# Performance work log

Measured on AMD Instinct MI355X. Metric: run time of the kernel, lower is better.

The kernel has to match this reference:

```python
import jax, jax.numpy as jnp
import numpy as np

EPS = 1e-9
# ((top,bottom),(left,right)) zero-pads for the 8 neighbor directions,
# matching torch nn.ZeroPad2d((l,r,t,b)) order gate1..gate8 in the source.
PADS = [((0, 2), (0, 2)), ((0, 2), (1, 1)), ((0, 2), (2, 0)),
        ((1, 1), (0, 2)), ((1, 1), (2, 0)),
        ((2, 0), (0, 2)), ((2, 0), (1, 1)), ((2, 0), (2, 0))]


def _pad8(x):
    # x: (B,H,W) -> (B,8,H+2,W+2): 8 directional zero-padded shifts
    return jnp.stack([jnp.pad(x, ((0, 0), tb, lr)) for tb, lr in PADS], axis=1)


def _affinity_normalization(guidance):
    # guidance: (B,8,H,W) -> gate_wb (B,8,H+2,W+2), gate_sum (B,H,W)
    gate_wb = jnp.stack(
        [jnp.pad(guidance[:, k], ((0, 0), tb, lr)) for k, (tb, lr) in enumerate(PADS)],
        axis=1)
    abs_weight = jnp.sum(jnp.abs(gate_wb), axis=1, keepdims=True)
    gate_wb = gate_wb / (abs_weight + EPS)
    gate_sum = jnp.sum(gate_wb, axis=1)[:, 1:-1, 1:-1]
    return gate_wb, gate_sum


def setup_inputs() -> dict:
    key = jax.random.key(0)
    k1, k2, k3, k4 = jax.random.split(key, 4)
    B, H, W = 2, 384, 1280
    guidance = jax.random.normal(k1, (B, 8, H, W), dtype=jnp.float32)
    blur_depth = jax.random.uniform(k2, (B, 1, H, W), dtype=jnp.float32) * 80.0
    valid = (jax.random.uniform(k3, (B, 1, H, W)) < 0.05).astype(jnp.float32)
    sparse_depth = valid * jax.random.uniform(k4, (B, 1, H, W), dtype=jnp.float32) * 80.0
    return {"guidance": guidance, "blur_depth": blur_depth,
            "sparse_depth": sparse_depth, "prop_time": 24}


def reference(guidance, blur_depth, sparse_depth, prop_time):
    # CSPN affinity-guided iterative propagation (norm_type='8sum')
    gate_wb, gate_sum = _affinity_normalization(guidance)
    raw = blur_depth[:, 0]                       # (B,H,W)
    sparse_mask = jnp.sign(sparse_depth[:, 0])   # (B,H,W), 1 where valid
    d = raw
    for _ in range(prop_time):
        # weighted sum over 8 padded neighbor shifts, then crop halo
        nws = jnp.sum(gate_wb * _pad8(d), axis=1)[:, 1:-1, 1:-1]
        d = (1.0 - gate_sum) * raw + nws
        d = (1.0 - sparse_mask) * d + sparse_mask * raw
    return d  # (B,H,W), matches result_depth.squeeze(1)
```

## Files before the change

### kernel.cpp

```cpp
#include <hip/hip_runtime.h>
#include <hip/hip_fp16.h>

static constexpr int Hh = 384;
static constexpr int Ww = 1280;
static constexpr int HW = Hh * Ww;
static constexpr int NPIX = 2 * HW;
static constexpr int TILE_I = 24;
static constexpr int TILE_J = 40;
static constexpr int S_STEPS = 8;
static constexpr int RI = TILE_I + 2 * S_STEPS;
static constexpr int RJ = TILE_J + 2 * S_STEPS;
static constexpr int RR = RI * RJ;
static constexpr int II = RI - 2;
static constexpr int IJ = RJ - 2;
static constexpr int NPAIR_ROW = IJ / 2;
static constexpr int NPAIR = II * NPAIR_ROW;
static constexpr int BLOCK = 512;
static constexpr int PPQ = (RR + BLOCK - 1) / BLOCK;
static constexpr int PPR = (NPAIR + BLOCK - 1) / BLOCK;
static constexpr int TI_T = Hh / TILE_I;
static constexpr int TJ_T = Ww / TILE_J;
static constexpr int GRID = 2 * TI_T * TJ_T;
static constexpr int NXCD = 8;
static constexpr int CHUNK = GRID / NXCD;
static constexpr float EPSF = 1e-9f;

static constexpr int DI[8] = { 1, 1, 1, 0, 0, -1, -1, -1 };
static constexpr int DJ[8] = { 1, 0, -1, 1, -1, 1, 0, -1 };

static __device__ __forceinline__ int iclamp(int v, int lo, int hi) {
    return min(max(v, lo), hi);
}

template <bool FIRST>
__global__ __launch_bounds__(BLOCK, 4)
void mega(
    const float* __restrict__ g,
    const float* blur,
    const float* __restrict__ sparse,
    const float* din,
    float* __restrict__ dout)
{
    __shared__ float sd[2][RR];

    const int tid = threadIdx.x;
    int bx = ((int)blockIdx.x % NXCD) * CHUNK + (int)blockIdx.x / NXCD;
    const int tj = bx % TJ_T; bx /= TJ_T;
    const int ti = bx % TI_T;
    const int b  = bx / TI_T;
    const int oi = ti * TILE_I - S_STEPS;
    const int oj = tj * TILE_J - S_STEPS;

    const float* blurb = blur + (size_t)b * HW;
    const float* dinb  = (FIRST ? blur : din) + (size_t)b * HW;
    const float* gb    = g + (size_t)b * 8 * HW;

#pragma unroll
    for (int q = 0; q < PPQ; q++) {
        int p = tid + q * BLOCK;
        if (p < RR) {
            int ri = p / RJ, rj = p - ri * RJ;
            int gi = iclamp(oi + ri, 0, Hh - 1);
            int gj = iclamp(oj + rj, 0, Ww - 1);
            sd[0][p] = dinb[gi * Ww + gj];
        }
    }

    __half2 wp[PPR][8];
    float2  Cc[PPR];
    int     pr[PPR];
#pragma unroll
    for (int q = 0; q < PPR; q++) {
        int pi = tid + q * BLOCK;
        if (pi < NPAIR) {
            int r0 = pi / NPAIR_ROW;
            int c0 = pi - r0 * NPAIR_ROW;
            int ri = 1 + r0;
            int rj = 1 + 2 * c0;
            int p  = ri * RJ + rj;
            int rngr = min(ri, RI - 1 - ri);
            int rng0 = min(rngr, min(rj,     RJ - 1 - rj));
            int rng1 = min(rngr, min(rj + 1, RJ - 2 - rj));
            pr[q] = p | (max(rng0, rng1) << 16);
            float Cv[2], wv[2][8];
#pragma unroll
            for (int x = 0; x < 2; x++) {
                int gi = iclamp(oi + ri, 0, Hh - 1);
                int gj = iclamp(oj + rj + x, 0, Ww - 1);
                float v[8];
                float a = EPSF;
#pragma unroll
                for (int k = 0; k < 8; k++) {
                    int ii = gi + DI[k], jj = gj + DJ[k];
                    float gv = 0.0f;
                    if (ii >= 0 && ii < Hh && jj >= 0 && jj < Ww)
                        gv = gb[k * HW + ii * Ww + jj];
                    v[k] = gv;
                    a += fabsf(gv);
                }
                float inv = 1.0f / a, gs = 0.0f;
#pragma unroll
                for (int k = 0; k < 8; k++) { v[k] *= inv; gs += v[k]; }
                int idx = gi * Ww + gj;
                float rawv = blurb[idx];
                bool m = sparse[b * HW + idx] > 0.0f;
                Cv[x] = m ? rawv : (1.0f - gs) * rawv;
#pragma unroll
                for (int k = 0; k < 8; k++) wv[x][k] = m ? 0.0f : v[k];
            }
            Cc[q] = make_float2(Cv[0], Cv[1]);
#pragma unroll
            for (int k = 0; k < 8; k++)
                wp[q][k] = __halves2half2(__float2half(wv[0][k]),
                                          __float2half(wv[1][k]));
        } else {
            pr[q] = 0;
            Cc[q] = make_float2(0.0f, 0.0f);
#pragma unroll
            for (int k = 0; k < 8; k++)
                wp[q][k] = __halves2half2(__float2half(0.0f), __float2half(0.0f));
        }
    }
    __syncthreads();

    int cur = 0;
#pragma unroll 1
    for (int s = 1; s < S_STEPS; ++s) {
        const float* s0 = sd[cur];
        float* s1 = sd[cur ^ 1];
#pragma unroll
        for (int q = 0; q < PPR; q++) {
            if ((pr[q] >> 16) >= s) {
                int p = pr[q] & 0xffff;
                float2 uA = *(const float2*)(s0 + p - RJ - 1);
                float2 uB = *(const float2*)(s0 + p - RJ + 1);
                float2 mA = *(const float2*)(s0 + p - 1);
                float2 mB = *(const float2*)(s0 + p + 1);
                float2 dA = *(const float2*)(s0 + p + RJ - 1);
                float2 dB = *(const float2*)(s0 + p + RJ + 1);
                float ax = Cc[q].x, ay = Cc[q].y;
                ax = fmaf(__low2float (wp[q][0]), dB.x, ax);
                ay = fmaf(__high2float(wp[q][0]), dB.y, ay);
                ax = fmaf(__low2float (wp[q][1]), dA.y, ax);
                ay = fmaf(__high2float(wp[q][1]), dB.x, ay);
                ax = fmaf(__low2float (wp[q][2]), dA.x, ax);
                ay = fmaf(__high2float(wp[q][2]), dA.y, ay);
                ax = fmaf(__low2float (wp[q][3]), mB.x, ax);
                ay = fmaf(__high2float(wp[q][3]), mB.y, ay);
                ax = fmaf(__low2float (wp[q][4]), mA.x, ax);
                ay = fmaf(__high2float(wp[q][4]), mA.y, ay);
                ax = fmaf(__low2float (wp[q][5]), uB.x, ax);
                ay = fmaf(__high2float(wp[q][5]), uB.y, ay);
                ax = fmaf(__low2float (wp[q][6]), uA.y, ax);
                ay = fmaf(__high2float(wp[q][6]), uB.x, ay);
                ax = fmaf(__low2float (wp[q][7]), uA.x, ax);
                ay = fmaf(__high2float(wp[q][7]), uA.y, ay);
                s1[p]     = ax;
                s1[p + 1] = ay;
            }
        }
        __syncthreads();
        cur ^= 1;
    }

    const float* s0 = sd[cur];
#pragma unroll
    for (int q = 0; q < PPR; q++) {
        if ((pr[q] >> 16) >= S_STEPS) {
            int p = pr[q] & 0xffff;
            float2 uA = *(const float2*)(s0 + p - RJ - 1);
            float2 uB = *(const float2*)(s0 + p - RJ + 1);
            float2 mA = *(const float2*)(s0 + p - 1);
            float2 mB = *(const float2*)(s0 + p + 1);
            float2 dA = *(const float2*)(s0 + p + RJ - 1);
            float2 dB = *(const float2*)(s0 + p + RJ + 1);
            float ax = Cc[q].x, ay = Cc[q].y;
            ax = fmaf(__low2float (wp[q][0]), dB.x, ax);
            ay = fmaf(__high2float(wp[q][0]), dB.y, ay);
            ax = fmaf(__low2float (wp[q][1]), dA.y, ax);
            ay = fmaf(__high2float(wp[q][1]), dB.x, ay);
            ax = fmaf(__low2float (wp[q][2]), dA.x, ax);
            ay = fmaf(__high2float(wp[q][2]), dA.y, ay);
            ax = fmaf(__low2float (wp[q][3]), mB.x, ax);
            ay = fmaf(__high2float(wp[q][3]), mB.y, ay);
            ax = fmaf(__low2float (wp[q][4]), mA.x, ax);
            ay = fmaf(__high2float(wp[q][4]), mA.y, ay);
            ax = fmaf(__low2float (wp[q][5]), uB.x, ax);
            ay = fmaf(__high2float(wp[q][5]), uB.y, ay);
            ax = fmaf(__low2float (wp[q][6]), uA.y, ax);
            ay = fmaf(__high2float(wp[q][6]), uB.x, ay);
            ax = fmaf(__low2float (wp[q][7]), uA.x, ax);
            ay = fmaf(__high2float(wp[q][7]), uA.y, ay);
            int ri = p / RJ, rj = p - ri * RJ;
            int gbase = b * HW + (oi + ri) * Ww + (oj + rj);
            if (rj >= S_STEPS && rj < RJ - S_STEPS)
                dout[gbase]     = ax;
            if (rj + 1 >= S_STEPS && rj + 1 < RJ - S_STEPS)
                dout[gbase + 1] = ay;
        }
    }
}

extern "C" void kernel_launch(void* const* d_in, const int* in_sizes, int n_in,
                              void* d_out, int out_size, void* d_ws, size_t ws_size,
                              hipStream_t stream) {
    const float* guidance = (const float*)d_in[0];
    const float* blur     = (const float*)d_in[1];
    const float* sparse   = (const float*)d_in[2];
    float* out = (float*)d_out;

    char* ws = (char*)d_ws;
    float* bufA = (float*)ws;
    float* bufB = bufA + NPIX;

    mega<true ><<<GRID, BLOCK, 0, stream>>>(guidance, blur, sparse, nullptr, bufA);
    mega<false><<<GRID, BLOCK, 0, stream>>>(guidance, blur, sparse, bufA, bufB);
    mega<false><<<GRID, BLOCK, 0, stream>>>(guidance, blur, sparse, bufB, out);
}
```

Measured before the change: 149.2 us.

## Precompute normalized affinity weights once in a separate kernel and enlarge tiles

```diff
diff --git a/kernel.cpp b/kernel.cpp
--- a/kernel.cpp
+++ b/kernel.cpp
@@ -5,7 +5,7 @@
 static constexpr int Ww = 1280;
 static constexpr int HW = Hh * Ww;
 static constexpr int NPIX = 2 * HW;
-static constexpr int TILE_I = 24;
+static constexpr int TILE_I = 32;
 static constexpr int TILE_J = 40;
 static constexpr int S_STEPS = 8;
 static constexpr int RI = TILE_I + 2 * S_STEPS;
@@ -25,19 +25,56 @@
 static constexpr int CHUNK = GRID / NXCD;
 static constexpr float EPSF = 1e-9f;
 
-static constexpr int DI[8] = { 1, 1, 1, 0, 0, -1, -1, -1 };
-static constexpr int DJ[8] = { 1, 0, -1, 1, -1, 1, 0, -1 };
+__device__ __constant__ int DI_c[8] = { 1, 1, 1, 0, 0, -1, -1, -1 };
+__device__ __constant__ int DJ_c[8] = { 1, 0, -1, 1, -1, 1, 0, -1 };
 
 static __device__ __forceinline__ int iclamp(int v, int lo, int hi) {
     return min(max(v, lo), hi);
 }
 
+__global__ void affinity_norm(const float* __restrict__ g,
+                              const float* __restrict__ raw,
+                              const float* __restrict__ sparse,
+                              __half* __restrict__ wbuf,
+                              float* __restrict__ cbuf) {
+    int idx = blockIdx.x * blockDim.x + threadIdx.x;
+    if (idx >= NPIX) return;
+    int b = idx / HW;
+    int r = idx - b * HW;
+    int i = r / Ww;
+    int j = r - i * Ww;
+
+    const float* gb = g + (size_t)b * 8 * HW;
+    float v[8];
+    float a = EPSF;
+#pragma unroll
+    for (int k = 0; k < 8; k++) {
+        int ii = i + DI_c[k], jj = j + DJ_c[k];
+        float gv = 0.0f;
+        if (ii >= 0 && ii < Hh && jj >= 0 && jj < Ww)
+            gv = gb[k * HW + ii * Ww + jj];
+        v[k] = gv;
+        a += fabsf(gv);
+    }
+    float inv = 1.0f / a, gs = 0.0f;
+#pragma unroll
+    for (int k = 0; k < 8; k++) { v[k] *= inv; gs += v[k]; }
+
+    float rawv = raw[idx];
+    bool m = sparse[idx] > 0.0f;
+    cbuf[idx] = m ? rawv : (1.0f - gs) * rawv;
+    __half wv[8];
+#pragma unroll
+    for (int k = 0; k < 8; k++) wv[k] = __float2half(m ? 0.0f : v[k]);
+    *(float4*)(wbuf + (size_t)idx * 8) = *(const float4*)wv;
+}
+
 template <bool FIRST>
-__global__ __launch_bounds__(BLOCK, 4)
+__global__ __launch_bounds__(BLOCK, 3)
 void mega(
-    const float* __restrict__ g,
+    const __half* __restrict__ wbuf,
+    const float* __restrict__ cbuf,
     const float* blur,
-    const float* __restrict__ sparse,
     const float* din,
     float* __restrict__ dout)
 {
@@ -51,9 +88,7 @@
     const int oi = ti * TILE_I - S_STEPS;
     const int oj = tj * TILE_J - S_STEPS;
 
-    const float* blurb = blur + (size_t)b * HW;
-    const float* dinb  = (FIRST ? blur : din) + (size_t)b * HW;
-    const float* gb    = g + (size_t)b * 8 * HW;
+    const float* dinb = (FIRST ? blur : din) + (size_t)b * HW;
 
 #pragma unroll
     for (int q = 0; q < PPQ; q++) {
@@ -82,37 +117,19 @@
             int rng0 = min(rngr, min(rj,     RJ - 1 - rj));
             int rng1 = min(rngr, min(rj + 1, RJ - 2 - rj));
             pr[q] = p | (max(rng0, rng1) << 16);
-            float Cv[2], wv[2][8];
-#pragma unroll
-            for (int x = 0; x < 2; x++) {
-                int gi = iclamp(oi + ri, 0, Hh - 1);
-                int gj = iclamp(oj + rj + x, 0, Ww - 1);
-                float v[8];
-                float a = EPSF;
-#pragma unroll
-                for (int k = 0; k < 8; k++) {
-                    int ii = gi + DI[k], jj = gj + DJ[k];
-                    float gv = 0.0f;
-                    if (ii >= 0 && ii < Hh && jj >= 0 && jj < Ww)
-                        gv = gb[k * HW + ii * Ww + jj];
-                    v[k] = gv;
-                    a += fabsf(gv);
-                }
-                float inv = 1.0f / a, gs = 0.0f;
-#pragma unroll
-                for (int k = 0; k < 8; k++) { v[k] *= inv; gs += v[k]; }
-                int idx = gi * Ww + gj;
-                float rawv = blurb[idx];
-                bool m = sparse[b * HW + idx] > 0.0f;
-                Cv[x] = m ? rawv : (1.0f - gs) * rawv;
-#pragma unroll
-                for (int k = 0; k < 8; k++) wv[x][k] = m ? 0.0f : v[k];
-            }
-            Cc[q] = make_float2(Cv[0], Cv[1]);
+            int gi = iclamp(oi + ri, 0, Hh - 1);
+            int gj0 = iclamp(oj + rj,     0, Ww - 1);
+            int gj1 = iclamp(oj + rj + 1, 0, Ww - 1);
+            int idx0 = b * HW + gi * Ww + gj0;
+            int idx1 = b * HW + gi * Ww + gj1;
+            float4 wA = *(const float4*)(wbuf + (size_t)idx0 * 8);
+            float4 wB = *(const float4*)(wbuf + (size_t)idx1 * 8);
+            const __half* ha = (const __half*)&wA;
+            const __half* hb = (const __half*)&wB;
 #pragma unroll
             for (int k = 0; k < 8; k++)
-                wp[q][k] = __halves2half2(__float2half(wv[0][k]),
-                                          __float2half(wv[1][k]));
+                wp[q][k] = __halves2half2(ha[k], hb[k]);
+            Cc[q] = make_float2(cbuf[idx0], cbuf[idx1]);
         } else {
             pr[q] = 0;
             Cc[q] = make_float2(0.0f, 0.0f);
@@ -212,8 +229,14 @@
     char* ws = (char*)d_ws;
     float* bufA = (float*)ws;
     float* bufB = bufA + NPIX;
-
-    mega<true ><<<GRID, BLOCK, 0, stream>>>(guidance, blur, sparse, nullptr, bufA);
-    mega<false><<<GRID, BLOCK, 0, stream>>>(guidance, blur, sparse, bufA, bufB);
-    mega<false><<<GRID, BLOCK, 0, stream>>>(guidance, blur, sparse, bufB, out);
-}
+    __half* wbuf = (__half*)(bufB + NPIX);
+    float*  cbuf = (float*)(wbuf + (size_t)NPIX * 8);
+
+    const int threads = 256;
+    const int blocks = (NPIX + threads - 1) / threads;
+    affinity_norm<<<blocks, threads, 0, stream>>>(guidance, blur, sparse, wbuf, cbuf);
+
+    mega<true ><<<GRID, BLOCK, 0, stream>>>(wbuf, cbuf, blur, nullptr, bufA);
+    mega<false><<<GRID, BLOCK, 0, stream>>>(wbuf, cbuf, nullptr, bufA, bufB);
+    mega<false><<<GRID, BLOCK, 0, stream>>>(wbuf, cbuf, nullptr, bufB, out);
+}
```

New measurement: 134.1 us. 1.11x faster.
